# Optimization experiments

Hardware: AMD Instinct MI355X
Metric: run time of the kernel (lower is better)

## Reference

```python
import jax, jax.numpy as jnp
import numpy as np

N_DST = 25000
E = 400000
DN = 128   # dim_node
DE = 128   # dim_edge
DT = 128   # dim_time
DO = 128   # dim_out
H = 2      # num_head


def setup_inputs() -> dict:
    key = jax.random.key(0)
    ks = jax.random.split(key, 10)
    sc = 0.05
    node_h = jax.random.normal(ks[0], (N_DST + E, DN), jnp.float32)
    edge_f = jax.random.normal(ks[1], (E, DE), jnp.float32)
    dt = jax.random.uniform(ks[2], (E,), jnp.float32) * 100.0
    dst_idx = jax.random.randint(ks[3], (E,), 0, N_DST)
    # TimeEncode: Linear(1, dim_time) with w initialized to 1/10**linspace(0,9)
    time_w = jnp.asarray(1.0 / 10 ** np.linspace(0, 9, DT, dtype=np.float32))
    time_b = jnp.zeros((DT,), jnp.float32)
    Wq = jax.random.normal(ks[4], (DO, DN + DT), jnp.float32) * sc
    bq = jnp.zeros((DO,), jnp.float32)
    Wk = jax.random.normal(ks[5], (DO, DN + DE + DT), jnp.float32) * sc
    bk = jnp.zeros((DO,), jnp.float32)
    Wv = jax.random.normal(ks[6], (DO, DN + DE + DT), jnp.float32) * sc
    bv = jnp.zeros((DO,), jnp.float32)
    Wout = jax.random.normal(ks[7], (DO, DN + DO), jnp.float32) * sc
    bout = jnp.zeros((DO,), jnp.float32)
    gamma = jnp.ones((DO,), jnp.float32)
    beta = jnp.zeros((DO,), jnp.float32)
    return dict(node_h=node_h, edge_f=edge_f, dt=dt, dst_idx=dst_idx,
                time_w=time_w, time_b=time_b, Wq=Wq, bq=bq, Wk=Wk, bk=bk,
                Wv=Wv, bv=bv, Wout=Wout, bout=bout, gamma=gamma, beta=beta)


def reference(node_h, edge_f, dt, dst_idx, time_w, time_b,
              Wq, bq, Wk, bk, Wv, bv, Wout, bout, gamma, beta):
    num_dst = node_h.shape[0] - edge_f.shape[0]
    num_edges = edge_f.shape[0]
    tgt = node_h[:num_dst]            # [N, DN] target node embeddings
    src = node_h[num_dst:]            # [E, DN] per-edge source embeddings

    # TimeEncode: cos(w * dt + b)
    time_feats = jnp.cos(dt[:, None] * time_w[None, :] + time_b)          # [E, DT]
    zero_time = jnp.broadcast_to(jnp.cos(time_b), (num_dst, time_b.shape[0]))

    Qn = jnp.concatenate([tgt, zero_time], axis=1) @ Wq.T + bq            # [N, DO]
    kv_in = jnp.concatenate([src, edge_f, time_feats], axis=1)            # [E, DN+DE+DT]
    K = kv_in @ Wk.T + bk                                                 # [E, DO]
    V = kv_in @ Wv.T + bv                                                 # [E, DO]
    Q = Qn[dst_idx]                                                       # gather per edge

    d_head = Q.shape[1] // H
    Qh = Q.reshape(num_edges, H, d_head)
    Kh = K.reshape(num_edges, H, d_head)
    Vh = V.reshape(num_edges, H, d_head)

    score = jnp.sum(Qh * Kh, axis=2)                                      # [E, H]
    score = jnp.where(score >= 0, score, 0.2 * score)                     # LeakyReLU(0.2)

    # edge_softmax: segmented softmax over incoming edges of each dst node
    m = jax.ops.segment_max(score, dst_idx, num_segments=num_dst)
    m = jnp.where(jnp.isfinite(m), m, 0.0)                                # empty segments
    e = jnp.exp(score - m[dst_idx])
    s = jax.ops.segment_sum(e, dst_idx, num_segments=num_dst)
    att = e / s[dst_idx]                                                  # [E, H]

    Vw = (Vh * att[:, :, None]).reshape(num_edges, -1)                    # [E, DO]
    h = jax.ops.segment_sum(Vw, dst_idx, num_segments=num_dst)            # scatter-sum

    rst = jnp.concatenate([h, tgt], axis=1) @ Wout.T + bout               # [N, DO]
    rst = jax.nn.relu(rst)
    mu = jnp.mean(rst, axis=-1, keepdims=True)
    var = jnp.var(rst, axis=-1, keepdims=True)
    return (rst - mu) / jnp.sqrt(var + 1e-5) * gamma + beta
```

## Files before the change

### kernel.cpp

```cpp
#include <hip/hip_runtime.h>

#define N_DST 25000
#define E_NUM 400000

typedef __bf16 bf16x8 __attribute__((ext_vector_type(8)));
typedef __bf16 bf16x4 __attribute__((ext_vector_type(4)));
typedef __bf16 bf16x2 __attribute__((ext_vector_type(2)));
typedef float  f32x4  __attribute__((ext_vector_type(4)));

__device__ __forceinline__ float fast_cos(float x) {
  float r = x * 0.15915494309189535f;
  r = r - floorf(r);
  return __builtin_amdgcn_cosf(r);
}

__device__ __forceinline__ void pack_frag(const float* __restrict__ W0,
    const float* __restrict__ W1, int stride, int NC, int idx, __bf16* __restrict__ out) {
  int lane = idx & 63, fid = idx >> 6;
  int nfw = NC >> 6;
  int perks = nfw << 2;
  int ks = fid / perks, rem = fid - ks * perks;
  int w = rem / nfw, nf = rem - w * nfw;
  int n = w * (NC >> 2) + nf * 16 + (lane & 15);
  int g = (ks << 2) + (lane >> 4);
  const float* src = (W1 && n >= 128) ? (W1 + (size_t)(n - 128) * stride)
                                      : (W0 + (size_t)n * stride);
  const float4* s4 = reinterpret_cast<const float4*>(src + g * 8);
  float4 lo = s4[0], hi = s4[1];
  bf16x8 b;
  b[0]=(__bf16)lo.x; b[1]=(__bf16)lo.y; b[2]=(__bf16)lo.z; b[3]=(__bf16)lo.w;
  b[4]=(__bf16)hi.x; b[5]=(__bf16)hi.y; b[6]=(__bf16)hi.z; b[7]=(__bf16)hi.w;
  reinterpret_cast<bf16x8*>(out)[idx] = b;
}

__global__ __launch_bounds__(256) void prep_kernel(
    const float* __restrict__ Wq, const float* __restrict__ bq, const float* __restrict__ tb,
    const float* __restrict__ Wk, const float* __restrict__ Wv, const float* __restrict__ Wout,
    const int* __restrict__ dsti,
    float* __restrict__ cq, __bf16* __restrict__ Bq_kv, __bf16* __restrict__ Bq_q,
    __bf16* __restrict__ Bq_out, int* __restrict__ counts) {
  int b = blockIdx.x, tid = threadIdx.x;
  if (b == 0) {
    if (tid < 128) {
      float s = bq[tid];
      for (int j = 0; j < 128; ++j) s += cosf(tb[j]) * Wq[tid * 256 + 128 + j];
      cq[tid] = s;
    }
    return;
  }
  b -= 1;
  if (b < 48) { pack_frag(Wk, Wv, 384, 256, b * 256 + tid, Bq_kv); return; }
  b -= 48;
  if (b < 8)  { pack_frag(Wq, nullptr, 256, 128, b * 256 + tid, Bq_q); return; }
  b -= 8;
  if (b < 16) { pack_frag(Wout, nullptr, 256, 128, b * 256 + tid, Bq_out); return; }
  b -= 16;
  int e = b * 256 + tid;
  if (e < E_NUM) atomicAdd(&counts[dsti[e]], 1);
}

__global__ __launch_bounds__(1024) void scanA_kernel(const int* __restrict__ counts,
    int* __restrict__ bsum) {
  __shared__ int wsum[16];
  int tid = threadIdx.x;
  int idx = blockIdx.x * 1024 + tid;
  int s = (idx < N_DST) ? counts[idx] : 0;
#pragma unroll
  for (int o = 32; o; o >>= 1) s += __shfl_xor(s, o);
  if ((tid & 63) == 0) wsum[tid >> 6] = s;
  __syncthreads();
  if (tid == 0) {
    int t = 0;
#pragma unroll
    for (int i = 0; i < 16; ++i) t += wsum[i];
    bsum[blockIdx.x] = t;
  }
}

__global__ void scanB_kernel(const int* __restrict__ bsum, int* __restrict__ boff) {
  if (threadIdx.x == 0) {
    int c = 0;
    for (int i = 0; i < 25; ++i) { boff[i] = c; c += bsum[i]; }
    boff[25] = c;
  }
}

__global__ __launch_bounds__(1024) void scanC_kernel(const int* __restrict__ counts,
    const int* __restrict__ boff, int* __restrict__ offs, int* __restrict__ cursor) {
  __shared__ int wpart[16];
  int tid = threadIdx.x, lane = tid & 63, wid = tid >> 6;
  int idx = blockIdx.x * 1024 + tid;
  int x = (idx < N_DST) ? counts[idx] : 0;
  int incl = x;
#pragma unroll
  for (int o = 1; o < 64; o <<= 1) {
    int y = __shfl_up(incl, o);
    if (lane >= o) incl += y;
  }
  if (lane == 63) wpart[wid] = incl;
  __syncthreads();
  if (wid == 0) {
    int v = (lane < 16) ? wpart[lane] : 0;
    int s = v;
#pragma unroll
    for (int o = 1; o < 16; o <<= 1) {
      int y = __shfl_up(s, o);
      if (lane >= o) s += y;
    }
    if (lane < 16) wpart[lane] = s;
  }
  __syncthreads();
  int woff = (wid > 0) ? wpart[wid - 1] : 0;
  int v = boff[blockIdx.x] + woff + incl - x;
  if (idx < N_DST) {
    offs[idx] = v;
    cursor[idx] = v;
  }
  if (idx == N_DST - 1) offs[N_DST] = v + x;
}

__global__ __launch_bounds__(256) void fill_kernel(const int* __restrict__ dsti,
    int* __restrict__ cursor, int* __restrict__ pos) {
  int e = blockIdx.x * 256 + threadIdx.x;
  if (e < E_NUM) {
    int d = dsti[e];
    int p = atomicAdd(&cursor[d], 1);
    pos[e] = p;
  }
}

__global__ __launch_bounds__(256, 4) void kv_kernel(
    const float* __restrict__ node_h, const float* __restrict__ edge_f,
    const float* __restrict__ dtp, const float* __restrict__ tw, const float* __restrict__ tb,
    const __bf16* __restrict__ Bq,
    const float* __restrict__ bk, const float* __restrict__ bv,
    const int* __restrict__ dsti, const int* __restrict__ pos,
    const float* __restrict__ Qn,
    __bf16* __restrict__ Vout, float* __restrict__ score)
{
  __shared__ __align__(16) char Ab[2][8192];
  __shared__ __align__(16) char Vlds[16384];
  __shared__ int Dlds[64];
  __shared__ int Plds[64];
  __shared__ float dts[64];
  __shared__ float twl[128];
  __shared__ float tbl[128];

  const int tid = threadIdx.x;
  const int e0 = blockIdx.x * 64;
  const int lane = tid & 63;
  const int w = tid >> 6;
  const int lrow = lane & 15;
  const int lk = lane >> 4;
  const int aswz = (lrow & 7) << 4;

  if (tid < 64) {
    Dlds[tid] = dsti[e0 + tid];
    Plds[tid] = pos[e0 + tid];
    dts[tid] = dtp[e0 + tid];
  } else if (tid < 192) {
    int j = tid - 64;
    twl[j] = tw[j];
    tbl[j] = tb[j];
  }
  __syncthreads();

  const int srow = tid >> 2;
  const int sq = tid & 3;
  const char* srcB = (const char*)(node_h + (size_t)(N_DST + e0) * 128);
  const char* edgB = (const char*)(edge_f + (size_t)e0 * 128);
  float4 st0, st1, st2, st3;

  auto issueL = [&](int t) {
    const char* base = (t < 2) ? (srcB + t * 256) : (edgB + (t - 2) * 256);
    const char* p = base + srow * 512 + sq * 64;
    asm volatile(
        "global_load_dwordx4 %0, %4, off\n\t"
        "global_load_dwordx4 %1, %4, off offset:16\n\t"
        "global_load_dwordx4 %2, %4, off offset:32\n\t"
        "global_load_dwordx4 %3, %4, off offset:48"
        : "=&v"(st0), "=&v"(st1), "=&v"(st2), "=&v"(st3)
        : "v"(p));
  };
  auto waitL = [&]() {
    asm volatile("s_waitcnt vmcnt(0)" ::: "memory");
    __builtin_amdgcn_sched_barrier(0);
  };
  auto writeA = [&](char* buf) {
    char* rb = buf + srow * 128;
    int sw = (srow & 7) << 4;
    float4 vv[4] = {st0, st1, st2, st3};
#pragma unroll
    for (int i = 0; i < 4; ++i) {
      bf16x4 b;
      b[0]=(__bf16)vv[i].x; b[1]=(__bf16)vv[i].y; b[2]=(__bf16)vv[i].z; b[3]=(__bf16)vv[i].w;
      *reinterpret_cast<bf16x4*>(rb + ((sq * 32 + i * 8) ^ sw)) = b;
    }
  };

  f32x4 acc[4][4];
#pragma unroll
  for (int mf = 0; mf < 4; ++mf)
#pragma unroll
    for (int nf = 0; nf < 4; ++nf)
      acc[mf][nf] = (f32x4){0.f, 0.f, 0.f, 0.f};

  const bf16x8* __restrict__ Bw = reinterpret_cast<const bf16x8*>(Bq) + (size_t)(w * 4) * 64 + lane;

  auto ktileM = [&](const char* buf, int t) {
#pragma unroll
    for (int ks = 0; ks < 2; ++ks) {
      int K32 = t * 2 + ks;
      bf16x8 b[4];
#pragma unroll
      for (int nf = 0; nf < 4; ++nf)
        b[nf] = Bw[((size_t)K32 * 16 + nf) * 64];
      bf16x8 a[4];
#pragma unroll
      for (int mf = 0; mf < 4; ++mf)
        a[mf] = *reinterpret_cast<const bf16x8*>(
            buf + (mf * 16 + lrow) * 128 + ((ks * 64 + lk * 16) ^ aswz));
#pragma unroll
      for (int nf = 0; nf < 4; ++nf)
#pragma unroll
        for (int mf = 0; mf < 4; ++mf)
          acc[mf][nf] = __builtin_amdgcn_mfma_f32_16x16x32_bf16(a[mf], b[nf], acc[mf][nf], 0, 0, 0);
    }
  };

  float dv[4];
#pragma unroll
  for (int mf = 0; mf < 4; ++mf) dv[mf] = dts[mf * 16 + lrow];

  auto ktileC = [&](int cs) {
    int K32 = 8 + cs;
    int J = cs * 32 + lk * 8;
    f32x4 w0 = *reinterpret_cast<const f32x4*>(twl + J);
    f32x4 w1 = *reinterpret_cast<const f32x4*>(twl + J + 4);
    f32x4 c0 = *reinterpret_cast<const f32x4*>(tbl + J);
    f32x4 c1 = *reinterpret_cast<const f32x4*>(tbl + J + 4);
    bf16x8 b[4];
#pragma unroll
    for (int nf = 0; nf < 4; ++nf)
      b[nf] = Bw[((size_t)K32 * 16 + nf) * 64];
#pragma unroll
    for (int mf = 0; mf < 4; ++mf) {
      float d = dv[mf];
      bf16x8 a;
#pragma unroll
      for (int j = 0; j < 4; ++j) {
        a[j] = (__bf16)fast_cos(d * w0[j] + c0[j]);
        a[4 + j] = (__bf16)fast_cos(d * w1[j] + c1[j]);
      }
#pragma unroll
      for (int nf = 0; nf < 4; ++nf)
        acc[mf][nf] = __builtin_amdgcn_mfma_f32_16x16x32_bf16(a, b[nf], acc[mf][nf], 0, 0, 0);
    }
  };

  issueL(0);
  waitL();
  writeA(Ab[0]);
  __syncthreads();
  issueL(1);
  ktileM(Ab[0], 0);
  waitL();
  writeA(Ab[1]);
  __syncthreads();
  issueL(2);
  ktileM(Ab[1], 1);
  waitL();
  writeA(Ab[0]);
  __syncthreads();
  issueL(3);
  ktileM(Ab[0], 2);
  waitL();
  writeA(Ab[1]);
  __syncthreads();
  ktileM(Ab[1], 3);
  ktileC(0); ktileC(1); ktileC(2); ktileC(3);

  if (w >= 2) {
#pragma unroll
    for (int nf = 0; nf < 4; ++nf) {
      int vcol = (w - 2) * 64 + nf * 16 + lrow;
      float bb = bv[vcol];
#pragma unroll
      for (int mf = 0; mf < 4; ++mf) {
#pragma unroll
        for (int r = 0; r < 4; ++r) {
          int row = mf * 16 + lk * 4 + r;
          *reinterpret_cast<__bf16*>(Vlds + row * 256 + ((vcol * 2) ^ ((row & 7) << 4))) =
              (__bf16)(acc[mf][nf][r] + bb);
        }
      }
    }
  } else {
    float bkv[4];
#pragma unroll
    for (int nf = 0; nf < 4; ++nf) bkv[nf] = bk[w * 64 + nf * 16 + lrow];
#pragma unroll
    for (int mf = 0; mf < 4; ++mf) {
#pragma unroll
      for (int r = 0; r < 4; ++r) {
        int row = mf * 16 + lk * 4 + r;
        const float* qrow = Qn + ((size_t)Dlds[row] << 7) + w * 64;
        float s = 0.f;
#pragma unroll
        for (int nf = 0; nf < 4; ++nf)
          s += (acc[mf][nf][r] + bkv[nf]) * qrow[nf * 16 + lrow];
        s += __shfl_xor(s, 1);
        s += __shfl_xor(s, 2);
        s += __shfl_xor(s, 4);
        s += __shfl_xor(s, 8);
        if (lrow == 0) {
          s = (s >= 0.f) ? s : 0.2f * s;
          score[((size_t)Plds[row] << 1) + w] = s;
        }
      }
    }
  }
  __syncthreads();
#pragma unroll
  for (int i = 0; i < 4; ++i) {
    int c = tid + i * 256;
    int r = c >> 4, cb = (c & 15) << 4;
    bf16x8 vv = *reinterpret_cast<const bf16x8*>(Vlds + r * 256 + (cb ^ ((r & 7) << 4)));
    *reinterpret_cast<bf16x8*>(Vout + (((size_t)Plds[r]) << 7) + (c & 15) * 8) = vv;
  }
}

template<int MODE>
__global__ __launch_bounds__(256, 4) void gemm_kernel(
    const float* __restrict__ A0, const float* __restrict__ A1,
    const float* __restrict__ dtp, const float* __restrict__ tw,
    const __bf16* __restrict__ Bq, const float* __restrict__ bias0,
    float* __restrict__ outF)
{
  constexpr int NC = 128;
  constexpr int NFRAGW = 2;
  __shared__ __align__(16) char Abuf[2][64 * 256];

  const int tid = threadIdx.x;
  const int e0 = blockIdx.x * 64;
  const int nv = min(64, N_DST - e0);
  const int srow = tid >> 5;
  const int sc4 = (tid & 31) << 2;

  const int lane = tid & 63;
  const int w = tid >> 6;
  const int nbase = w * (NC / 4);
  const int lrow = lane & 15;
  const int lk = lane >> 4;
  const int aswz = (lrow & 7) << 4;
  const bf16x8* __restrict__ Bw =
      reinterpret_cast<const bf16x8*>(Bq) + (size_t)(w * NFRAGW) * 64 + lane;

  f32x4 acc[4][NFRAGW];
#pragma unroll
  for (int mf = 0; mf < 4; ++mf)
#pragma unroll
    for (int nf = 0; nf < NFRAGW; ++nf)
      acc[mf][nf] = (f32x4){0.f, 0.f, 0.f, 0.f};

  auto issueA = [&](int t, float4 (&v)[8]) {
    const float* base = (t == 0) ? A0 : A1;
#pragma unroll
    for (int i = 0; i < 8; ++i) {
      int r = srow + i * 8;
      v[i] = (r < nv) ? *reinterpret_cast<const float4*>(base + (size_t)(e0 + r) * 128 + sc4)
                      : make_float4(0.f, 0.f, 0.f, 0.f);
    }
  };
  auto writeA = [&](char* buf, float4 (&v)[8]) {
#pragma unroll
    for (int i = 0; i < 8; ++i) {
      int r = srow + i * 8;
      bf16x4 b;
      b[0]=(__bf16)v[i].x; b[1]=(__bf16)v[i].y; b[2]=(__bf16)v[i].z; b[3]=(__bf16)v[i].w;
      *reinterpret_cast<bf16x4*>(buf + r * 256 + ((sc4 * 2) ^ ((r & 7) << 4))) = b;
    }
  };
  auto ktile = [&](const char* buf, int t) {
#pragma unroll
    for (int ks = 0; ks < 4; ++ks) {
      bf16x8 b[NFRAGW];
#pragma unroll
      for (int nf = 0; nf < NFRAGW; ++nf)
        b[nf] = Bw[((size_t)(t * 4 + ks) * 4 * NFRAGW + nf) * 64];
      bf16x8 a[4];
#pragma unroll
      for (int mf = 0; mf < 4; ++mf)
        a[mf] = *reinterpret_cast<const bf16x8*>(
            buf + (mf * 16 + lrow) * 256 + (((ks * 32 + lk * 8) * 2) ^ aswz));
#pragma unroll
      for (int nf = 0; nf < NFRAGW; ++nf)
#pragma unroll
        for (int mf = 0; mf < 4; ++mf)
          acc[mf][nf] = __builtin_amdgcn_mfma_f32_16x16x32_bf16(a[mf], b[nf], acc[mf][nf], 0, 0, 0);
    }
  };

  float4 v[8];
  issueA(0, v);
  writeA(Abuf[0], v);
  __syncthreads();
  if constexpr (MODE == 2) {
    issueA(1, v);
    ktile(Abuf[0], 0);
    writeA(Abuf[1], v);
    __syncthreads();
    ktile(Abuf[1], 1);
  } else {
    ktile(Abuf[0], 0);
  }

  if constexpr (MODE == 0) {
#pragma unroll
    for (int nf = 0; nf < NFRAGW; ++nf) {
      int col = nbase + nf * 16 + lrow;
      float bb = bias0[col];
#pragma unroll
      for (int mf = 0; mf < 4; ++mf) {
#pragma unroll
        for (int r = 0; r < 4; ++r) {
          int row = mf * 16 + lk * 4 + r;
          if (row < nv)
            outF[(size_t)(e0 + row) * 128 + col] = acc[mf][nf][r] + bb;
        }
      }
    }
  } else {
    const float* gammaP = dtp;
    const float* betaP = tw;
    float vals[NFRAGW][4][4];
#pragma unroll
    for (int nf = 0; nf < NFRAGW; ++nf) {
      float bb = bias0[nbase + nf * 16 + lrow];
#pragma unroll
      for (int mf = 0; mf < 4; ++mf)
#pragma unroll
        for (int r = 0; r < 4; ++r)
          vals[nf][mf][r] = fmaxf(acc[mf][nf][r] + bb, 0.f);
    }
    __syncthreads();
    float* sums = reinterpret_cast<float*>(Abuf[0]);
    float* sqs  = reinterpret_cast<float*>(Abuf[0]) + 256;
    float* stats = reinterpret_cast<float*>(Abuf[0]) + 512;
#pragma unroll
    for (int mf = 0; mf < 4; ++mf) {
#pragma unroll
      for (int r = 0; r < 4; ++r) {
        float s1 = vals[0][mf][r] + vals[1][mf][r];
        float s2 = vals[0][mf][r] * vals[0][mf][r] + vals[1][mf][r] * vals[1][mf][r];
#pragma unroll
        for (int o = 1; o < 16; o <<= 1) {
          s1 += __shfl_xor(s1, o);
          s2 += __shfl_xor(s2, o);
        }
        if (lrow == 0) {
          int row = mf * 16 + lk * 4 + r;
          sums[w * 64 + row] = s1;
          sqs[w * 64 + row] = s2;
        }
      }
    }
    __syncthreads();
    if (tid < 64) {
      float s = sums[tid] + sums[64 + tid] + sums[128 + tid] + sums[192 + tid];
      float q = sqs[tid] + sqs[64 + tid] + sqs[128 + tid] + sqs[192 + tid];
      float mean = s * (1.f / 128.f);
      float var = q * (1.f / 128.f) - mean * mean;
      stats[tid * 2] = mean;
      stats[tid * 2 + 1] = rsqrtf(var + 1e-5f);
    }
    __syncthreads();
#pragma unroll
    for (int nf = 0; nf < NFRAGW; ++nf) {
      int col = nbase + nf * 16 + lrow;
      float g = gammaP[col], bC = betaP[col];
#pragma unroll
      for (int mf = 0; mf < 4; ++mf) {
#pragma unroll
        for (int r = 0; r < 4; ++r) {
          int row = mf * 16 + lk * 4 + r;
          if (row < nv) {
            float mean = stats[row * 2], rs = stats[row * 2 + 1];
            outF[(size_t)(e0 + row) * 128 + col] = (vals[nf][mf][r] - mean) * rs * g + bC;
          }
        }
      }
    }
  }
}

__global__ __launch_bounds__(256) void agg_kernel(const int* __restrict__ offs,
    const float* __restrict__ score, const __bf16* __restrict__ V, float* __restrict__ h) {
  int d = blockIdx.x * 4 + (threadIdx.x >> 6);
  if (d >= N_DST) return;
  int lane = threadIdx.x & 63;
  int beg = offs[d], end = offs[d + 1];
  int n = end - beg;
  float m0 = -3.0e38f, m1 = -3.0e38f;
  for (int i = lane; i < n; i += 64) {
    float2 sc = *reinterpret_cast<const float2*>(score + 2 * (size_t)(beg + i));
    m0 = fmaxf(m0, sc.x); m1 = fmaxf(m1, sc.y);
  }
#pragma unroll
  for (int o = 32; o; o >>= 1) {
    m0 = fmaxf(m0, __shfl_xor(m0, o));
    m1 = fmaxf(m1, __shfl_xor(m1, o));
  }
  float s0 = 0.f, s1 = 0.f;
  for (int i = lane; i < n; i += 64) {
    float2 sc = *reinterpret_cast<const float2*>(score + 2 * (size_t)(beg + i));
    s0 += __expf(sc.x - m0); s1 += __expf(sc.y - m1);
  }
#pragma unroll
  for (int o = 32; o; o >>= 1) {
    s0 += __shfl_xor(s0, o);
    s1 += __shfl_xor(s1, o);
  }
  float inv0 = (n > 0) ? 1.f / s0 : 0.f;
  float inv1 = (n > 0) ? 1.f / s1 : 0.f;
  int q = lane >> 4, j = lane & 15;
  int hsel = j >> 3;
  float acc[8];
#pragma unroll
  for (int k2 = 0; k2 < 8; ++k2) acc[k2] = 0.f;
  for (int i0 = 0; i0 < n; i0 += 4) {
    int i = i0 + q;
    if (i < n) {
      size_t p = beg + i;
      float2 sc = *reinterpret_cast<const float2*>(score + 2 * p);
      float wgt = hsel ? __expf(sc.y - m1) * inv1 : __expf(sc.x - m0) * inv0;
      bf16x8 v = *reinterpret_cast<const bf16x8*>(V + (p << 7) + j * 8);
#pragma unroll
      for (int k2 = 0; k2 < 8; ++k2) acc[k2] += wgt * (float)v[k2];
    }
  }
#pragma unroll
  for (int k2 = 0; k2 < 8; ++k2) {
    acc[k2] += __shfl_xor(acc[k2], 16);
    acc[k2] += __shfl_xor(acc[k2], 32);
  }
  if (q == 0) {
    float4 lo = make_float4(acc[0], acc[1], acc[2], acc[3]);
    float4 hi = make_float4(acc[4], acc[5], acc[6], acc[7]);
    float* dst = h + ((size_t)d << 7) + j * 8;
    *reinterpret_cast<float4*>(dst) = lo;
    *reinterpret_cast<float4*>(dst + 4) = hi;
  }
}

extern "C" void kernel_launch(void* const* d_in, const int* in_sizes, int n_in,
                              void* d_out, int out_size, void* d_ws, size_t ws_size,
                              hipStream_t stream) {
  (void)in_sizes; (void)n_in; (void)out_size; (void)ws_size;
  const float* node_h = (const float*)d_in[0];
  const float* edge_f = (const float*)d_in[1];
  const float* dtp    = (const float*)d_in[2];
  const int*   dsti   = (const int*)d_in[3];
  const float* tw     = (const float*)d_in[4];
  const float* tb     = (const float*)d_in[5];
  const float* Wq     = (const float*)d_in[6];
  const float* bq     = (const float*)d_in[7];
  const float* Wk     = (const float*)d_in[8];
  const float* bk     = (const float*)d_in[9];
  const float* Wv     = (const float*)d_in[10];
  const float* bv     = (const float*)d_in[11];
  const float* Wout   = (const float*)d_in[12];
  const float* bout   = (const float*)d_in[13];
  const float* gamma  = (const float*)d_in[14];
  const float* beta   = (const float*)d_in[15];
  float* outp = (float*)d_out;

  size_t off = 0;
  auto take = [&](size_t nbytes) -> void* {
    void* r = (char*)d_ws + off;
    off += (nbytes + 255) & ~(size_t)255;
    return r;
  };
  __bf16* Bq_kv  = (__bf16*)take((size_t)12288 * 16);
  __bf16* Bq_q   = (__bf16*)take((size_t)2048 * 16);
  __bf16* Bq_out = (__bf16*)take((size_t)4096 * 16);
  float*  cq     = (float*)take(128 * 4);
  float*  Qn     = (float*)take((size_t)N_DST * 128 * 4);
  __bf16* Vbuf   = (__bf16*)take((size_t)E_NUM * 128 * 2);
  float*  score  = (float*)take((size_t)E_NUM * 2 * 4);
  int*    counts = (int*)take((size_t)N_DST * 4);
  int*    offs   = (int*)take((size_t)(N_DST + 1) * 4);
  int*    cursor = (int*)take((size_t)N_DST * 4);
  int*    pos    = (int*)take((size_t)E_NUM * 4);
  int*    bsum   = (int*)take(32 * 4);
  int*    boff   = (int*)take(32 * 4);
  float*  hbuf   = (float*)take((size_t)N_DST * 128 * 4);

  hipMemsetAsync(counts, 0, (size_t)N_DST * 4, stream);

  const int count_blocks = (E_NUM + 255) / 256;
  prep_kernel<<<1 + 48 + 8 + 16 + count_blocks, 256, 0, stream>>>(
      Wq, bq, tb, Wk, Wv, Wout, dsti, cq, Bq_kv, Bq_q, Bq_out, counts);

  gemm_kernel<0><<<(N_DST + 63) / 64, 256, 0, stream>>>(node_h, nullptr, nullptr, nullptr,
      Bq_q, cq, Qn);

  scanA_kernel<<<25, 1024, 0, stream>>>(counts, bsum);
  scanB_kernel<<<1, 64, 0, stream>>>(bsum, boff);
  scanC_kernel<<<25, 1024, 0, stream>>>(counts, boff, offs, cursor);
  fill_kernel<<<count_blocks, 256, 0, stream>>>(dsti, cursor, pos);

  kv_kernel<<<E_NUM / 64, 256, 0, stream>>>(node_h, edge_f, dtp, tw, tb,
      Bq_kv, bk, bv, dsti, pos, Qn, Vbuf, score);

  agg_kernel<<<(N_DST + 3) / 4, 256, 0, stream>>>(offs, score, Vbuf, hbuf);

  gemm_kernel<2><<<(N_DST + 63) / 64, 256, 0, stream>>>(hbuf, node_h, gamma, beta,
      Bq_out, bout, outp);
}
```

Baseline: 341.3 us.

## Process edges in dst-sorted order and fuse aggregation into output GEMM

```diff
diff --git a/kernel.cpp b/kernel.cpp
--- a/kernel.cpp
+++ b/kernel.cpp
@@ -5,7 +5,6 @@
 
 typedef __bf16 bf16x8 __attribute__((ext_vector_type(8)));
 typedef __bf16 bf16x4 __attribute__((ext_vector_type(4)));
-typedef __bf16 bf16x2 __attribute__((ext_vector_type(2)));
 typedef float  f32x4  __attribute__((ext_vector_type(4)));
 
 __device__ __forceinline__ float fast_cos(float x) {
@@ -120,12 +119,13 @@
 }
 
 __global__ __launch_bounds__(256) void fill_kernel(const int* __restrict__ dsti,
-    int* __restrict__ cursor, int* __restrict__ pos) {
+    int* __restrict__ cursor, int* __restrict__ elist, int* __restrict__ dsts) {
   int e = blockIdx.x * 256 + threadIdx.x;
   if (e < E_NUM) {
     int d = dsti[e];
     int p = atomicAdd(&cursor[d], 1);
-    pos[e] = p;
+    elist[p] = e;
+    dsts[p] = d;
   }
 }
 
@@ -134,14 +134,14 @@
     const float* __restrict__ dtp, const float* __restrict__ tw, const float* __restrict__ tb,
     const __bf16* __restrict__ Bq,
     const float* __restrict__ bk, const float* __restrict__ bv,
-    const int* __restrict__ dsti, const int* __restrict__ pos,
+    const int* __restrict__ elist, const int* __restrict__ dsts,
     const float* __restrict__ Qn,
     __bf16* __restrict__ Vout, float* __restrict__ score)
 {
   __shared__ __align__(16) char Ab[2][8192];
   __shared__ __align__(16) char Vlds[16384];
+  __shared__ int Elds[64];
   __shared__ int Dlds[64];
-  __shared__ int Plds[64];
   __shared__ float dts[64];
   __shared__ float twl[128];
   __shared__ float tbl[128];
@@ -155,9 +155,10 @@
   const int aswz = (lrow & 7) << 4;
 
   if (tid < 64) {
-    Dlds[tid] = dsti[e0 + tid];
-    Plds[tid] = pos[e0 + tid];
-    dts[tid] = dtp[e0 + tid];
+    int e = elist[e0 + tid];
+    Elds[tid] = e;
+    Dlds[tid] = dsts[e0 + tid];
+    dts[tid] = dtp[e];
   } else if (tid < 192) {
     int j = tid - 64;
     twl[j] = tw[j];
@@ -167,13 +168,13 @@
 
   const int srow = tid >> 2;
   const int sq = tid & 3;
-  const char* srcB = (const char*)(node_h + (size_t)(N_DST + e0) * 128);
-  const char* edgB = (const char*)(edge_f + (size_t)e0 * 128);
+  const int eidx = Elds[srow];
+  const char* sR = (const char*)(node_h + (size_t)(N_DST + eidx) * 128) + sq * 64;
+  const char* eR = (const char*)(edge_f + (size_t)eidx * 128) + sq * 64;
   float4 st0, st1, st2, st3;
 
   auto issueL = [&](int t) {
-    const char* base = (t < 2) ? (srcB + t * 256) : (edgB + (t - 2) * 256);
-    const char* p = base + srow * 512 + sq * 64;
+    const char* p = (t < 2) ? (sR + t * 256) : (eR + (t - 2) * 256);
     asm volatile(
         "global_load_dwordx4 %0, %4, off\n\t"
         "global_load_dwordx4 %1, %4, off offset:16\n\t"
@@ -315,7 +316,7 @@
         s += __shfl_xor(s, 8);
         if (lrow == 0) {
           s = (s >= 0.f) ? s : 0.2f * s;
-          score[((size_t)Plds[row] << 1) + w] = s;
+          score[((size_t)(e0 + row) << 1) + w] = s;
         }
       }
     }
@@ -326,230 +327,261 @@
     int c = tid + i * 256;
     int r = c >> 4, cb = (c & 15) << 4;
     bf16x8 vv = *reinterpret_cast<const bf16x8*>(Vlds + r * 256 + (cb ^ ((r & 7) << 4)));
-    *reinterpret_cast<bf16x8*>(Vout + (((size_t)Plds[r]) << 7) + (c & 15) * 8) = vv;
-  }
-}
-
-template<int MODE>
-__global__ __launch_bounds__(256, 4) void gemm_kernel(
-    const float* __restrict__ A0, const float* __restrict__ A1,
-    const float* __restrict__ dtp, const float* __restrict__ tw,
-    const __bf16* __restrict__ Bq, const float* __restrict__ bias0,
-    float* __restrict__ outF)
+    *reinterpret_cast<bf16x8*>(Vout + (((size_t)(e0 + r)) << 7) + (c & 15) * 8) = vv;
+  }
+}
+
+__global__ __launch_bounds__(256, 4) void q_kernel(
+    const float* __restrict__ A0, const __bf16* __restrict__ Bq,
+    const float* __restrict__ cq, float* __restrict__ outF)
 {
-  constexpr int NC = 128;
-  constexpr int NFRAGW = 2;
-  __shared__ __align__(16) char Abuf[2][64 * 256];
-
+  __shared__ __align__(16) char Abuf[64 * 256];
   const int tid = threadIdx.x;
   const int e0 = blockIdx.x * 64;
   const int nv = min(64, N_DST - e0);
   const int srow = tid >> 5;
   const int sc4 = (tid & 31) << 2;
-
   const int lane = tid & 63;
   const int w = tid >> 6;
-  const int nbase = w * (NC / 4);
+  const int nbase = w * 32;
   const int lrow = lane & 15;
   const int lk = lane >> 4;
   const int aswz = (lrow & 7) << 4;
   const bf16x8* __restrict__ Bw =
-      reinterpret_cast<const bf16x8*>(Bq) + (size_t)(w * NFRAGW) * 64 + lane;
-
-  f32x4 acc[4][NFRAGW];
+      reinterpret_cast<const bf16x8*>(Bq) + (size_t)(w * 2) * 64 + lane;
+
+  f32x4 acc[4][2];
 #pragma unroll
   for (int mf = 0; mf < 4; ++mf)
 #pragma unroll
-    for (int nf = 0; nf < NFRAGW; ++nf)
+    for (int nf = 0; nf < 2; ++nf)
       acc[mf][nf] = (f32x4){0.f, 0.f, 0.f, 0.f};
 
-  auto issueA = [&](int t, float4 (&v)[8]) {
-    const float* base = (t == 0) ? A0 : A1;
+#pragma unroll
+  for (int i = 0; i < 8; ++i) {
+    int r = srow + i * 8;
+    float4 v = (r < nv) ? *reinterpret_cast<const float4*>(A0 + (size_t)(e0 + r) * 128 + sc4)
+                        : make_float4(0.f, 0.f, 0.f, 0.f);
+    bf16x4 b;
+    b[0]=(__bf16)v.x; b[1]=(__bf16)v.y; b[2]=(__bf16)v.z; b[3]=(__bf16)v.w;
+    *reinterpret_cast<bf16x4*>(Abuf + r * 256 + ((sc4 * 2) ^ ((r & 7) << 4))) = b;
+  }
+  __syncthreads();
+
+#pragma unroll
+  for (int ks = 0; ks < 4; ++ks) {
+    bf16x8 b[2];
+#pragma unroll
+    for (int nf = 0; nf < 2; ++nf)
+      b[nf] = Bw[((size_t)ks * 8 + nf) * 64];
+    bf16x8 a[4];
+#pragma unroll
+    for (int mf = 0; mf < 4; ++mf)
+      a[mf] = *reinterpret_cast<const bf16x8*>(
+          Abuf + (mf * 16 + lrow) * 256 + (((ks * 32 + lk * 8) * 2) ^ aswz));
+#pragma unroll
+    for (int nf = 0; nf < 2; ++nf)
+#pragma unroll
+      for (int mf = 0; mf < 4; ++mf)
+        acc[mf][nf] = __builtin_amdgcn_mfma_f32_16x16x32_bf16(a[mf], b[nf], acc[mf][nf], 0, 0, 0);
+  }
+
+#pragma unroll
+  for (int nf = 0; nf < 2; ++nf) {
+    int col = nbase + nf * 16 + lrow;
+    float bb = cq[col];
+#pragma unroll
+    for (int mf = 0; mf < 4; ++mf) {
+#pragma unroll
+      for (int r = 0; r < 4; ++r) {
+        int row = mf * 16 + lk * 4 + r;
+        if (row < nv)
+          outF[(size_t)(e0 + row) * 128 + col] = acc[mf][nf][r] + bb;
+      }
+    }
+  }
+}
+
+__global__ __launch_bounds__(256, 4) void out_kernel(
+    const float* __restrict__ node_h, const int* __restrict__ offs,
+    const float* __restrict__ score, const __bf16* __restrict__ V,
+    const float* __restrict__ gamma, const float* __restrict__ beta,
+    const __bf16* __restrict__ Bq, const float* __restrict__ bout,
+    float* __restrict__ outp)
+{
+  __shared__ __align__(16) char Ah[64 * 256];
+  __shared__ __align__(16) char At[64 * 256];
+  const int tid = threadIdx.x;
+  const int d0 = blockIdx.x * 64;
+  const int nv = min(64, N_DST - d0);
+  const int lane = tid & 63;
+  const int w = tid >> 6;
+  const int lrow = lane & 15;
+  const int lk = lane >> 4;
+  const int aswz = (lrow & 7) << 4;
+
+  {
+    int srow = tid >> 5;
+    int sc4 = (tid & 31) << 2;
 #pragma unroll
     for (int i = 0; i < 8; ++i) {
       int r = srow + i * 8;
-      v[i] = (r < nv) ? *reinterpret_cast<const float4*>(base + (size_t)(e0 + r) * 128 + sc4)
-                      : make_float4(0.f, 0.f, 0.f, 0.f);
-    }
-  };
-  auto writeA = [&](char* buf, float4 (&v)[8]) {
-#pragma unroll
-    for (int i = 0; i < 8; ++i) {
-      int r = srow + i * 8;
+      float4 v = (r < nv) ? *reinterpret_cast<const float4*>(node_h + (size_t)(d0 + r) * 128 + sc4)
+                          : make_float4(0.f, 0.f, 0.f, 0.f);
       bf16x4 b;
-      b[0]=(__bf16)v[i].x; b[1]=(__bf16)v[i].y; b[2]=(__bf16)v[i].z; b[3]=(__bf16)v[i].w;
-      *reinterpret_cast<bf16x4*>(buf + r * 256 + ((sc4 * 2) ^ ((r & 7) << 4))) = b;
-    }
-  };
-  auto ktile = [&](const char* buf, int t) {
+      b[0]=(__bf16)v.x; b[1]=(__bf16)v.y; b[2]=(__bf16)v.z; b[3]=(__bf16)v.w;
+      *reinterpret_cast<bf16x4*>(At + r * 256 + ((sc4 * 2) ^ ((r & 7) << 4))) = b;
+    }
+  }
+
+  for (int k = 0; k < 16; ++k) {
+    int row = w * 16 + k;
+    int d = d0 + row;
+    if (d < N_DST) {
+      int beg = offs[d], end = offs[d + 1];
+      int n = end - beg;
+      float m0 = -3.0e38f, m1 = -3.0e38f;
+      for (int i = lane; i < n; i += 64) {
+        float2 sc = *reinterpret_cast<const float2*>(score + 2 * (size_t)(beg + i));
+        m0 = fmaxf(m0, sc.x); m1 = fmaxf(m1, sc.y);
+      }
+#pragma unroll
+      for (int o = 32; o; o >>= 1) {
+        m0 = fmaxf(m0, __shfl_xor(m0, o));
+        m1 = fmaxf(m1, __shfl_xor(m1, o));
+      }
+      float s0 = 0.f, s1 = 0.f;
+      for (int i = lane; i < n; i += 64) {
+        float2 sc = *reinterpret_cast<const float2*>(score + 2 * (size_t)(beg + i));
+        s0 += __expf(sc.x - m0); s1 += __expf(sc.y - m1);
+      }
+#pragma unroll
+      for (int o = 32; o; o >>= 1) {
+        s0 += __shfl_xor(s0, o);
+        s1 += __shfl_xor(s1, o);
+      }
+      float inv0 = (n > 0) ? 1.f / s0 : 0.f;
+      float inv1 = (n > 0) ? 1.f / s1 : 0.f;
+      int q = lane >> 4, j = lane & 15;
+      int hsel = j >> 3;
+      float acc[8];
+#pragma unroll
+      for (int k2 = 0; k2 < 8; ++k2) acc[k2] = 0.f;
+      for (int i0 = 0; i0 < n; i0 += 4) {
+        int i = i0 + q;
+        if (i < n) {
+          size_t p = beg + i;
+          float2 sc = *reinterpret_cast<const float2*>(score + 2 * p);
+          float wgt = hsel ? __expf(sc.y - m1) * inv1 : __expf(sc.x - m0) * inv0;
+          bf16x8 v = *reinterpret_cast<const bf16x8*>(V + (p << 7) + j * 8);
+#pragma unroll
+          for (int k2 = 0; k2 < 8; ++k2) acc[k2] += wgt * (float)v[k2];
+        }
+      }
+#pragma unroll
+      for (int k2 = 0; k2 < 8; ++k2) {
+        acc[k2] += __shfl_xor(acc[k2], 16);
+        acc[k2] += __shfl_xor(acc[k2], 32);
+      }
+      if (q == 0) {
+        bf16x8 hb;
+#pragma unroll
+        for (int k2 = 0; k2 < 8; ++k2) hb[k2] = (__bf16)acc[k2];
+        *reinterpret_cast<bf16x8*>(Ah + row * 256 + ((j * 16) ^ ((row & 7) << 4))) = hb;
+      }
+    }
+  }
+  __syncthreads();
+
+  const bf16x8* __restrict__ Bw =
+      reinterpret_cast<const bf16x8*>(Bq) + (size_t)(w * 2) * 64 + lane;
+  f32x4 acc[4][2];
+#pragma unroll
+  for (int mf = 0; mf < 4; ++mf)
+#pragma unroll
+    for (int nf = 0; nf < 2; ++nf)
+      acc[mf][nf] = (f32x4){0.f, 0.f, 0.f, 0.f};
+
+#pragma unroll
+  for (int t = 0; t < 2; ++t) {
+    const char* buf = (t == 0) ? Ah : At;
 #pragma unroll
     for (int ks = 0; ks < 4; ++ks) {
-      bf16x8 b[NFRAGW];
-#pragma unroll
-      for (int nf = 0; nf < NFRAGW; ++nf)
-        b[nf] = Bw[((size_t)(t * 4 + ks) * 4 * NFRAGW + nf) * 64];
+      bf16x8 b[2];
+#pragma unroll
+      for (int nf = 0; nf < 2; ++nf)
+        b[nf] = Bw[((size_t)(t * 4 + ks) * 8 + nf) * 64];
       bf16x8 a[4];
 #pragma unroll
       for (int mf = 0; mf < 4; ++mf)
         a[mf] = *reinterpret_cast<const bf16x8*>(
             buf + (mf * 16 + lrow) * 256 + (((ks * 32 + lk * 8) * 2) ^ aswz));
 #pragma unroll
-      for (int nf = 0; nf < NFRAGW; ++nf)
+      for (int nf = 0; nf < 2; ++nf)
 #pragma unroll
         for (int mf = 0; mf < 4; ++mf)
           acc[mf][nf] = __builtin_amdgcn_mfma_f32_16x16x32_bf16(a[mf], b[nf], acc[mf][nf], 0, 0, 0);
     }
-  };
-
-  float4 v[8];
-  issueA(0, v);
-  writeA(Abuf[0], v);
-  __syncthreads();
-  if constexpr (MODE == 2) {
-    issueA(1, v);
-    ktile(Abuf[0], 0);
-    writeA(Abuf[1], v);
-    __syncthreads();
-    ktile(Abuf[1], 1);
-  } else {
-    ktile(Abuf[0], 0);
-  }
-
-  if constexpr (MODE == 0) {
-#pragma unroll
-    for (int nf = 0; nf < NFRAGW; ++nf) {
-      int col = nbase + nf * 16 + lrow;
-      float bb = bias0[col];
-#pragma unroll
-      for (int mf = 0; mf < 4; ++mf) {
-#pragma unroll
-        for (int r = 0; r < 4; ++r) {
-          int row = mf * 16 + lk * 4 + r;
-          if (row < nv)
-            outF[(size_t)(e0 + row) * 128 + col] = acc[mf][nf][r] + bb;
+  }
+
+  const int nbase = w * 32;
+  float vals[2][4][4];
+#pragma unroll
+  for (int nf = 0; nf < 2; ++nf) {
+    float bb = bout[nbase + nf * 16 + lrow];
+#pragma unroll
+    for (int mf = 0; mf < 4; ++mf)
+#pragma unroll
+      for (int r = 0; r < 4; ++r)
+        vals[nf][mf][r] = fmaxf(acc[mf][nf][r] + bb, 0.f);
+  }
+  __syncthreads();
+  float* sums = reinterpret_cast<float*>(Ah);
+  float* sqs  = reinterpret_cast<float*>(Ah) + 256;
+  float* stats = reinterpret_cast<float*>(Ah) + 512;
+#pragma unroll
+  for (int mf = 0; mf < 4; ++mf) {
+#pragma unroll
+    for (int r = 0; r < 4; ++r) {
+      float s1 = vals[0][mf][r] + vals[1][mf][r];
+      float s2 = vals[0][mf][r] * vals[0][mf][r] + vals[1][mf][r] * vals[1][mf][r];
+#pragma unroll
+      for (int o = 1; o < 16; o <<= 1) {
+        s1 += __shfl_xor(s1, o);
+        s2 += __shfl_xor(s2, o);
+      }
+      if (lrow == 0) {
+        int row = mf * 16 + lk * 4 + r;
+        sums[w * 64 + row] = s1;
+        sqs[w * 64 + row] = s2;
+      }
+    }
+  }
+  __syncthreads();
+  if (tid < 64) {
+    float s = sums[tid] + sums[64 + tid] + sums[128 + tid] + sums[192 + tid];
+    float q = sqs[tid] + sqs[64 + tid] + sqs[128 + tid] + sqs[192 + tid];
+    float mean = s * (1.f / 128.f);
+    float var = q * (1.f / 128.f) - mean * mean;
+    stats[tid * 2] = mean;
+    stats[tid * 2 + 1] = rsqrtf(var + 1e-5f);
+  }
+  __syncthreads();
+#pragma unroll
+  for (int nf = 0; nf < 2; ++nf) {
+    int col = nbase + nf * 16 + lrow;
+    float g = gamma[col], bC = beta[col];
+#pragma unroll
+    for (int mf = 0; mf < 4; ++mf) {
+#pragma unroll
+      for (int r = 0; r < 4; ++r) {
+        int row = mf * 16 + lk * 4 + r;
+        if (row < nv) {
+          float mean = stats[row * 2], rs = stats[row * 2 + 1];
+          outp[(size_t)(d0 + row) * 128 + col] = (vals[nf][mf][r] - mean) * rs * g + bC;
         }
       }
     }
-  } else {
-    const float* gammaP = dtp;
-    const float* betaP = tw;
-    float vals[NFRAGW][4][4];
-#pragma unroll
-    for (int nf = 0; nf < NFRAGW; ++nf) {
-      float bb = bias0[nbase + nf * 16 + lrow];
-#pragma unroll
-      for (int mf = 0; mf < 4; ++mf)
-#pragma unroll
-        for (int r = 0; r < 4; ++r)
-          vals[nf][mf][r] = fmaxf(acc[mf][nf][r] + bb, 0.f);
-    }
-    __syncthreads();
-    float* sums = reinterpret_cast<float*>(Abuf[0]);
-    float* sqs  = reinterpret_cast<float*>(Abuf[0]) + 256;
-    float* stats = reinterpret_cast<float*>(Abuf[0]) + 512;
-#pragma unroll
-    for (int mf = 0; mf < 4; ++mf) {
-#pragma unroll
-      for (int r = 0; r < 4; ++r) {
-        float s1 = vals[0][mf][r] + vals[1][mf][r];
-        float s2 = vals[0][mf][r] * vals[0][mf][r] + vals[1][mf][r] * vals[1][mf][r];
-#pragma unroll
-        for (int o = 1; o < 16; o <<= 1) {
-          s1 += __shfl_xor(s1, o);
-          s2 += __shfl_xor(s2, o);
-        }
-        if (lrow == 0) {
-          int row = mf * 16 + lk * 4 + r;
-          sums[w * 64 + row] = s1;
-          sqs[w * 64 + row] = s2;
-        }
-      }
-    }
-    __syncthreads();
-    if (tid < 64) {
-      float s = sums[tid] + sums[64 + tid] + sums[128 + tid] + sums[192 + tid];
-      float q = sqs[tid] + sqs[64 + tid] + sqs[128 + tid] + sqs[192 + tid];
-      float mean = s * (1.f / 128.f);
-      float var = q * (1.f / 128.f) - mean * mean;
-      stats[tid * 2] = mean;
-      stats[tid * 2 + 1] = rsqrtf(var + 1e-5f);
-    }
-    __syncthreads();
-#pragma unroll
-    for (int nf = 0; nf < NFRAGW; ++nf) {
-      int col = nbase + nf * 16 + lrow;
-      float g = gammaP[col], bC = betaP[col];
-#pragma unroll
-      for (int mf = 0; mf < 4; ++mf) {
-#pragma unroll
-        for (int r = 0; r < 4; ++r) {
-          int row = mf * 16 + lk * 4 + r;
-          if (row < nv) {
-            float mean = stats[row * 2], rs = stats[row * 2 + 1];
-            outF[(size_t)(e0 + row) * 128 + col] = (vals[nf][mf][r] - mean) * rs * g + bC;
-          }
-        }
-      }
-    }
-  }
-}
-
-__global__ __launch_bounds__(256) void agg_kernel(const int* __restrict__ offs,
-    const float* __restrict__ score, const __bf16* __restrict__ V, float* __restrict__ h) {
-  int d = blockIdx.x * 4 + (threadIdx.x >> 6);
-  if (d >= N_DST) return;
-  int lane = threadIdx.x & 63;
-  int beg = offs[d], end = offs[d + 1];
-  int n = end - beg;
-  float m0 = -3.0e38f, m1 = -3.0e38f;
-  for (int i = lane; i < n; i += 64) {
-    float2 sc = *reinterpret_cast<const float2*>(score + 2 * (size_t)(beg + i));
-    m0 = fmaxf(m0, sc.x); m1 = fmaxf(m1, sc.y);
-  }
-#pragma unroll
-  for (int o = 32; o; o >>= 1) {
-    m0 = fmaxf(m0, __shfl_xor(m0, o));
-    m1 = fmaxf(m1, __shfl_xor(m1, o));
-  }
-  float s0 = 0.f, s1 = 0.f;
-  for (int i = lane; i < n; i += 64) {
-    float2 sc = *reinterpret_cast<const float2*>(score + 2 * (size_t)(beg + i));
-    s0 += __expf(sc.x - m0); s1 += __expf(sc.y - m1);
-  }
-#pragma unroll
-  for (int o = 32; o; o >>= 1) {
-    s0 += __shfl_xor(s0, o);
-    s1 += __shfl_xor(s1, o);
-  }
-  float inv0 = (n > 0) ? 1.f / s0 : 0.f;
-  float inv1 = (n > 0) ? 1.f / s1 : 0.f;
-  int q = lane >> 4, j = lane & 15;
-  int hsel = j >> 3;
-  float acc[8];
-#pragma unroll
-  for (int k2 = 0; k2 < 8; ++k2) acc[k2] = 0.f;
-  for (int i0 = 0; i0 < n; i0 += 4) {
-    int i = i0 + q;
-    if (i < n) {
-      size_t p = beg + i;
-      float2 sc = *reinterpret_cast<const float2*>(score + 2 * p);
-      float wgt = hsel ? __expf(sc.y - m1) * inv1 : __expf(sc.x - m0) * inv0;
-      bf16x8 v = *reinterpret_cast<const bf16x8*>(V + (p << 7) + j * 8);
-#pragma unroll
-      for (int k2 = 0; k2 < 8; ++k2) acc[k2] += wgt * (float)v[k2];
-    }
-  }
-#pragma unroll
-  for (int k2 = 0; k2 < 8; ++k2) {
-    acc[k2] += __shfl_xor(acc[k2], 16);
-    acc[k2] += __shfl_xor(acc[k2], 32);
-  }
-  if (q == 0) {
-    float4 lo = make_float4(acc[0], acc[1], acc[2], acc[3]);
-    float4 hi = make_float4(acc[4], acc[5], acc[6], acc[7]);
-    float* dst = h + ((size_t)d << 7) + j * 8;
-    *reinterpret_cast<float4*>(dst) = lo;
-    *reinterpret_cast<float4*>(dst + 4) = hi;
   }
 }
 
@@ -591,10 +623,10 @@
   int*    counts = (int*)take((size_t)N_DST * 4);
   int*    offs   = (int*)take((size_t)(N_DST + 1) * 4);
   int*    cursor = (int*)take((size_t)N_DST * 4);
-  int*    pos    = (int*)take((size_t)E_NUM * 4);
+  int*    elist  = (int*)take((size_t)E_NUM * 4);
+  int*    dsts   = (int*)take((size_t)E_NUM * 4);
   int*    bsum   = (int*)take(32 * 4);
   int*    boff   = (int*)take(32 * 4);
-  float*  hbuf   = (float*)take((size_t)N_DST * 128 * 4);
 
   hipMemsetAsync(counts, 0, (size_t)N_DST * 4, stream);
 
@@ -602,19 +634,16 @@
   prep_kernel<<<1 + 48 + 8 + 16 + count_blocks, 256, 0, stream>>>(
       Wq, bq, tb, Wk, Wv, Wout, dsti, cq, Bq_kv, Bq_q, Bq_out, counts);
 
-  gemm_kernel<0><<<(N_DST + 63) / 64, 256, 0, stream>>>(node_h, nullptr, nullptr, nullptr,
-      Bq_q, cq, Qn);
+  q_kernel<<<(N_DST + 63) / 64, 256, 0, stream>>>(node_h, Bq_q, cq, Qn);
 
   scanA_kernel<<<25, 1024, 0, stream>>>(counts, bsum);
   scanB_kernel<<<1, 64, 0, stream>>>(bsum, boff);
   scanC_kernel<<<25, 1024, 0, stream>>>(counts, boff, offs, cursor);
-  fill_kernel<<<count_blocks, 256, 0, stream>>>(dsti, cursor, pos);
+  fill_kernel<<<count_blocks, 256, 0, stream>>>(dsti, cursor, elist, dsts);
 
   kv_kernel<<<E_NUM / 64, 256, 0, stream>>>(node_h, edge_f, dtp, tw, tb,
-      Bq_kv, bk, bv, dsti, pos, Qn, Vbuf, score);
-
-  agg_kernel<<<(N_DST + 3) / 4, 256, 0, stream>>>(offs, score, Vbuf, hbuf);
-
-  gemm_kernel<2><<<(N_DST + 63) / 64, 256, 0, stream>>>(hbuf, node_h, gamma, beta,
-      Bq_out, bout, outp);
-}
+      Bq_kv, bk, bv, elist, dsts, Qn, Vbuf, score);
+
+  out_kernel<<<(N_DST + 63) / 64, 256, 0, stream>>>(node_h, offs, score, Vbuf,
+      gamma, beta, Bq_out, bout, outp);
+}
```

Result: slower. 404.3 us (+18.5%).
